# Kernel tuning notes

Hardware: AMD Instinct MI355X
Metric: run time of the kernel (lower is better)

Reference implementation:

```python
import jax, jax.numpy as jnp
from jax import lax
import numpy as np

NDIM = 256
BATCH = 65536
NROT = NDIM * (NDIM - 1) // 2  # comb(ndim, 2) = 32640


def _givens_mat(rots, ii, jj, ndim):
    """Product G_last @ ... @ G_1 of Givens rotations in combinations order.

    Left-multiplying by G(i, j, theta) only modifies rows i and j, so we apply
    each rotation as a rank-2 row update instead of a full matmul (same math
    as the original `plane_rot_mat @ mat` loop).
    """
    def step(mat, carry):
        i, j, th = carry
        c = jnp.cos(th)
        s = jnp.sin(th)
        ri = mat[i]
        rj = mat[j]
        mat = mat.at[i].set(c * ri - s * rj)
        mat = mat.at[j].set(s * ri + c * rj)
        return mat, None

    mat0 = jnp.eye(ndim, dtype=jnp.complex64)
    mat, _ = lax.scan(step, mat0, (ii, jj, rots))
    return mat


def setup_inputs() -> dict:
    key = jax.random.key(0)
    k1, k2, k3, k4 = jax.random.split(key, 4)
    x = jax.random.normal(k1, (BATCH, NDIM), dtype=jnp.float32)
    rots1 = 0.1 * jax.random.normal(k2, (NROT,), dtype=jnp.float32)
    phases = 0.1 * jax.random.normal(k3, (NDIM,), dtype=jnp.float32)
    rots2 = 0.1 * jax.random.normal(k4, (NROT,), dtype=jnp.float32)
    return {"x": x, "rots1": rots1, "phases": phases, "rots2": rots2}


def reference(x, rots1, phases, rots2):
    ndim = x.shape[1]
    # np.triu_indices(ndim, 1) enumerates (i, j) pairs in the same row-major
    # order as itertools.combinations(range(ndim), 2).
    ii_np, jj_np = np.triu_indices(ndim, k=1)
    ii = jnp.asarray(ii_np, dtype=jnp.int32)
    jj = jnp.asarray(jj_np, dtype=jnp.int32)

    # vector_norm: row-wise L2 normalization
    xn = x / jnp.linalg.norm(x, axis=1, keepdims=True)
    xc = xn.astype(jnp.complex64)

    # rot1: y = x @ M1.T with M1 = G_last @ ... @ G_1
    M1 = _givens_mat(rots1, ii, jj, ndim)
    y = xc @ M1.T

    # phase_transforms: x @ diag(exp(i*phases)) == elementwise phase multiply
    y = y * jnp.exp(1j * phases)

    # rot2
    M2 = _givens_mat(rots2, ii, jj, ndim)
    y = y @ M2.T

    # measure: |.|^2
    return jnp.abs(y) ** 2
```

## Files before the change

kernel.cpp:

```cpp
#include <hip/hip_runtime.h>
#include <stdint.h>
#include <math.h>

#define NDIM 256
#define BATCH 65536
#define NROT 32640

typedef float  f32x4 __attribute__((ext_vector_type(4)));
typedef short  s16x8 __attribute__((ext_vector_type(8)));
typedef unsigned int u32x4 __attribute__((ext_vector_type(4)));
typedef unsigned int u32x2 __attribute__((ext_vector_type(2)));

static __device__ __forceinline__ unsigned short f2bf(float f) {
    unsigned int u = __float_as_uint(f);
    u += 0x7fffu + ((u >> 16) & 1u);
    return (unsigned short)(u >> 16);
}
static __device__ __forceinline__ float bf2f(unsigned short h) {
    return __uint_as_float(((unsigned)h) << 16);
}

static __device__ __forceinline__ void split4(f32x4 v, u32x2* hi, u32x2* lo) {
    unsigned short h[4], l[4];
    #pragma unroll
    for (int i = 0; i < 4; i++) {
        h[i] = f2bf(v[i]);
        l[i] = f2bf(v[i] - bf2f(h[i]));
    }
    *hi = (u32x2){ (unsigned)h[0] | ((unsigned)h[1] << 16),
                   (unsigned)h[2] | ((unsigned)h[3] << 16) };
    *lo = (u32x2){ (unsigned)l[0] | ((unsigned)l[1] << 16),
                   (unsigned)l[2] | ((unsigned)l[3] << 16) };
}
static __device__ __forceinline__ void split8(const float* v, u32x4* hi, u32x4* lo) {
    unsigned short h[8], l[8];
    #pragma unroll
    for (int i = 0; i < 8; i++) {
        h[i] = f2bf(v[i]);
        l[i] = f2bf(v[i] - bf2f(h[i]));
    }
    *hi = (u32x4){ (unsigned)h[0] | ((unsigned)h[1] << 16),
                   (unsigned)h[2] | ((unsigned)h[3] << 16),
                   (unsigned)h[4] | ((unsigned)h[5] << 16),
                   (unsigned)h[6] | ((unsigned)h[7] << 16) };
    *lo = (u32x4){ (unsigned)l[0] | ((unsigned)l[1] << 16),
                   (unsigned)l[2] | ((unsigned)l[3] << 16),
                   (unsigned)l[4] | ((unsigned)l[5] << 16),
                   (unsigned)l[6] | ((unsigned)l[7] << 16) };
}

static __device__ __forceinline__ int sweep_bound(int k, int pblk) {
    int target = k * (NROT / pblk);
    int best = 0, bd = 0x7fffffff;
    for (int i = 0; i <= 256; i += 4) {
        int pre = i * 255 - (i * (i - 1)) / 2;
        int d = pre - target; d = (d < 0) ? -d : d;
        if (d < bd) { bd = d; best = i; }
    }
    return best;
}

__global__ __launch_bounds__(256) void k_cs(const float* __restrict__ r1,
                                            const float* __restrict__ r2,
                                            float2* __restrict__ cs) {
    int i = blockIdx.x * 256 + threadIdx.x;
    float th = (i < NROT) ? r1[i] : r2[i - NROT];
    float sv, cv; sincosf(th, &sv, &cv);
    cs[i] = make_float2(cv, sv);
}

__global__ __launch_bounds__(64) void k_blocks(const float2* __restrict__ cs,
                                               float* __restrict__ bmats, int pblk) {
    __shared__ float colb[264 * 64];
    __shared__ float2 csb[256 * 4];
    __shared__ float2 tri[24 * 6];

    const int t = threadIdx.x;
    const int bid = blockIdx.x;
    const int chunk = bid & 3;
    const int b = (bid >> 2) % pblk;
    const int set = (bid >> 2) / pblk;
    const int col0 = chunk * 64;
    const float2* cst = cs + (size_t)set * NROT;

    const int s0 = sweep_bound(b, pblk);
    const int s1 = sweep_bound(b + 1, pblk);
    const int ngroups = (s1 - s0) >> 2;

    {
        const f32x4 z = {0.f, 0.f, 0.f, 0.f};
        #pragma unroll 11
        for (int q = 0; q < 66; q++)
            *(f32x4*)&colb[(q * 64 + t) * 4] = z;
        colb[(col0 + t) * 64 + t] = 1.0f;
    }

    for (int k = t; k < ngroups * 6; k += 64) {
        int g = k / 6, q = k - g * 6;
        int a  = (q < 3) ? 0 : ((q < 5) ? 1 : 2);
        int bb = (q < 3) ? (q + 1) : ((q < 5) ? (q - 1) : 3);
        int m0 = s0 + g * 4;
        int m = m0 + a;
        int base = m * 255 - (m * (m - 1)) / 2;
        tri[k] = cst[base - m - 1 + m0 + bb];
    }

    for (int g = 0; g < ngroups; g++) {
        const int m0 = s0 + g * 4;
        int off[4];
        #pragma unroll
        for (int a = 0; a < 4; a++) {
            int m = m0 + a;
            int base = m * 255 - (m * (m - 1)) / 2;
            off[a] = base - m - 1;
        }
        const int n_j = 252 - m0;
        const int n_p = (n_j > 0) ? ((n_j + 7) & ~7) : 0;

        {
            const int kmax = n_p * 4;
            #pragma unroll 4
            for (int it = 0; it < 16; it++) {
                int k = t + it * 64;
                if (k < kmax) {
                    int jj = k >> 2, a = k & 3;
                    int j = m0 + 4 + jj;
                    csb[k] = (j < 256) ? cst[off[a] + j] : make_float2(1.f, 0.f);
                }
            }
        }

        float u0 = colb[(m0 + 0) * 64 + t];
        float u1 = colb[(m0 + 1) * 64 + t];
        float u2 = colb[(m0 + 2) * 64 + t];
        float u3 = colb[(m0 + 3) * 64 + t];

        {
            float2 cv; float nr;
            cv = tri[g * 6 + 0]; nr = cv.y * u0 + cv.x * u1; u0 = cv.x * u0 - cv.y * u1; u1 = nr;
            cv = tri[g * 6 + 1]; nr = cv.y * u0 + cv.x * u2; u0 = cv.x * u0 - cv.y * u2; u2 = nr;
            cv = tri[g * 6 + 2]; nr = cv.y * u0 + cv.x * u3; u0 = cv.x * u0 - cv.y * u3; u3 = nr;
            cv = tri[g * 6 + 3]; nr = cv.y * u1 + cv.x * u2; u1 = cv.x * u1 - cv.y * u2; u2 = nr;
            cv = tri[g * 6 + 4]; nr = cv.y * u1 + cv.x * u3; u1 = cv.x * u1 - cv.y * u3; u3 = nr;
            cv = tri[g * 6 + 5]; nr = cv.y * u2 + cv.x * u3; u2 = cv.x * u2 - cv.y * u3; u3 = nr;
        }

        if (n_p > 0) {
            float rbuf[8];
            #pragma unroll
            for (int p = 0; p < 8; p++)
                rbuf[p] = colb[(m0 + 4 + p) * 64 + t];
            for (int c = 0; c < n_p; c += 8) {
                #pragma unroll
                for (int p = 0; p < 8; p++) {
                    const int j = m0 + 4 + c + p;
                    float r = rbuf[p];
                    int jn = j + 8; jn = (jn < 263) ? jn : 263;
                    rbuf[p] = colb[jn * 64 + t];
                    float2 a0 = csb[(c + p) * 4 + 0];
                    float2 a1 = csb[(c + p) * 4 + 1];
                    float2 a2 = csb[(c + p) * 4 + 2];
                    float2 a3 = csb[(c + p) * 4 + 3];
                    float nr;
                    nr = a0.y * u0 + a0.x * r; u0 = a0.x * u0 - a0.y * r; r = nr;
                    nr = a1.y * u1 + a1.x * r; u1 = a1.x * u1 - a1.y * r; r = nr;
                    nr = a2.y * u2 + a2.x * r; u2 = a2.x * u2 - a2.y * r; r = nr;
                    nr = a3.y * u3 + a3.x * r; u3 = a3.x * u3 - a3.y * r; r = nr;
                    colb[j * 64 + t] = r;
                }
            }
        }
        colb[(m0 + 0) * 64 + t] = u0;
        colb[(m0 + 1) * 64 + t] = u1;
        colb[(m0 + 2) * 64 + t] = u2;
        colb[(m0 + 3) * 64 + t] = u3;
    }

    float* outm = bmats + (size_t)(set * pblk + b) * 65536;
    for (int r = 0; r < 256; r++)
        outm[(size_t)r * 256 + col0 + t] = colb[r * 64 + t];
}

__global__ __launch_bounds__(256) void k_combine(const float* __restrict__ src,
                                                 float* __restrict__ dst,
                                                 int half, int pblk,
                                                 const float* __restrict__ xg,
                                                 unsigned short* __restrict__ xbf) {
    const int by = blockIdx.y;
    const int tid = threadIdx.x;

    if (by >= 2 * half) {
        const int id = (by - 2 * half) * 16 + blockIdx.x;
        const int w = tid >> 6, lane = tid & 63;
        const int r0 = id * 64;
        #pragma unroll 2
        for (int p = 0; p < 16; p++) {
            int row = r0 + p * 4 + w;
            f32x4 v = *(const f32x4*)&xg[(size_t)row * 256 + lane * 4];
            float s = v[0] * v[0] + v[1] * v[1] + v[2] * v[2] + v[3] * v[3];
            #pragma unroll
            for (int off = 32; off; off >>= 1) s += __shfl_xor(s, off, 64);
            float sc = 1.0f / sqrtf(s);
            unsigned short h0 = f2bf(v[0] * sc), h1 = f2bf(v[1] * sc);
            unsigned short h2 = f2bf(v[2] * sc), h3 = f2bf(v[3] * sc);
            u32x2 pk = { (unsigned)h0 | ((unsigned)h1 << 16),
                         (unsigned)h2 | ((unsigned)h3 << 16) };
            *(u32x2*)&xbf[(size_t)row * 256 + lane * 4] = pk;
        }
        return;
    }

    const int set = by / half, pidx = by % half;
    const int stride = pblk / (2 * half);
    const int s0A = sweep_bound((2 * pidx + 1) * stride, pblk);
    const float* Am = src + (size_t)(set * 2 * half + 2 * pidx + 1) * 65536;
    const float* Bm = src + (size_t)(set * 2 * half + 2 * pidx) * 65536;
    float* Dm = dst + (size_t)(set * half + pidx) * 65536;
    const int tr = blockIdx.x >> 2, tc = blockIdx.x & 3;

    if (tr * 64 + 64 <= s0A) {
        #pragma unroll
        for (int it = 0; it < 4; it++) {
            int flat = tid + it * 256;
            int r = flat >> 4, c4 = flat & 15;
            size_t idx = (size_t)(tr * 64 + r) * 256 + tc * 64 + c4 * 4;
            *(f32x4*)&Dm[idx] = *(const f32x4*)&Bm[idx];
        }
        return;
    }
    const int kb0 = (tr * 64 >= s0A) ? (s0A >> 5) : 0;

    __shared__ unsigned short Ahi[64 * 40], Alo[64 * 40];
    __shared__ unsigned short Bhi[64 * 40], Blo[64 * 40];

    const int lane = tid & 63, w = tid >> 6;
    const int mh = (w >> 1) * 32, nh = (w & 1) * 32;
    const int l15 = lane & 15, lq = lane >> 4;
    const int bn = tid & 63, bkq = tid >> 6;

    f32x4 acc[2][2];
    #pragma unroll
    for (int i = 0; i < 2; i++)
        #pragma unroll
        for (int j = 0; j < 2; j++) acc[i][j] = (f32x4){0.f, 0.f, 0.f, 0.f};

    for (int kb = kb0; kb < 8; kb++) {
        __syncthreads();
        #pragma unroll
        for (int it = 0; it < 2; it++) {
            int flat = tid + it * 256;
            int r = flat >> 3, c4 = flat & 7;
            f32x4 v = *(const f32x4*)&Am[(size_t)(tr * 64 + r) * 256 + kb * 32 + c4 * 4];
            u32x2 hi, lo; split4(v, &hi, &lo);
            *(u32x2*)&Ahi[r * 40 + c4 * 4] = hi;
            *(u32x2*)&Alo[r * 40 + c4 * 4] = lo;
        }
        {
            float bv[8];
            #pragma unroll
            for (int i = 0; i < 8; i++)
                bv[i] = Bm[(size_t)(kb * 32 + bkq * 8 + i) * 256 + tc * 64 + bn];
            u32x4 hi, lo; split8(bv, &hi, &lo);
            *(u32x4*)&Bhi[bn * 40 + bkq * 8] = hi;
            *(u32x4*)&Blo[bn * 40 + bkq * 8] = lo;
        }
        __syncthreads();
        s16x8 ah[2], al[2], bh[2], bl[2];
        #pragma unroll
        for (int tm = 0; tm < 2; tm++) {
            ah[tm] = *(const s16x8*)&Ahi[(mh + tm * 16 + l15) * 40 + lq * 8];
            al[tm] = *(const s16x8*)&Alo[(mh + tm * 16 + l15) * 40 + lq * 8];
        }
        #pragma unroll
        for (int tn = 0; tn < 2; tn++) {
            bh[tn] = *(const s16x8*)&Bhi[(nh + tn * 16 + l15) * 40 + lq * 8];
            bl[tn] = *(const s16x8*)&Blo[(nh + tn * 16 + l15) * 40 + lq * 8];
        }
        #pragma unroll
        for (int tm = 0; tm < 2; tm++)
            #pragma unroll
            for (int tn = 0; tn < 2; tn++) {
                acc[tm][tn] = __builtin_amdgcn_mfma_f32_16x16x32_bf16(ah[tm], bh[tn], acc[tm][tn], 0, 0, 0);
                acc[tm][tn] = __builtin_amdgcn_mfma_f32_16x16x32_bf16(ah[tm], bl[tn], acc[tm][tn], 0, 0, 0);
                acc[tm][tn] = __builtin_amdgcn_mfma_f32_16x16x32_bf16(al[tm], bh[tn], acc[tm][tn], 0, 0, 0);
            }
    }
    #pragma unroll
    for (int tm = 0; tm < 2; tm++)
        #pragma unroll
        for (int tn = 0; tn < 2; tn++)
            #pragma unroll
            for (int r = 0; r < 4; r++)
                Dm[(size_t)(tr * 64 + mh + tm * 16 + lq * 4 + r) * 256
                   + tc * 64 + nh + tn * 16 + l15] = acc[tm][tn][r];
}

__global__ __launch_bounds__(256) void k_abt(const float* __restrict__ mats,
                                             const float* __restrict__ phases,
                                             unsigned short* __restrict__ abt) {
    const float* Am = mats + 65536;
    const float* Bm = mats;
    const int v = blockIdx.y;
    const int tr = blockIdx.x >> 2, tc = blockIdx.x & 3;
    const int tid = threadIdx.x;

    __shared__ unsigned short Ahi[64 * 40], Alo[64 * 40];
    __shared__ unsigned short Bhi[64 * 40], Blo[64 * 40];

    const int lane = tid & 63, w = tid >> 6;
    const int mh = (w >> 1) * 32, nh = (w & 1) * 32;
    const int l15 = lane & 15, lq = lane >> 4;
    const int bn = tid & 63, bkq = tid >> 6;

    f32x4 acc[2][2];
    #pragma unroll
    for (int i = 0; i < 2; i++)
        #pragma unroll
        for (int j = 0; j < 2; j++) acc[i][j] = (f32x4){0.f, 0.f, 0.f, 0.f};

    for (int kb = 0; kb < 8; kb++) {
        __syncthreads();
        #pragma unroll
        for (int it = 0; it < 2; it++) {
            int flat = tid + it * 256;
            int r = flat >> 3, c4 = flat & 7;
            f32x4 vv = *(const f32x4*)&Am[(size_t)(tr * 64 + r) * 256 + kb * 32 + c4 * 4];
            u32x2 hi, lo; split4(vv, &hi, &lo);
            *(u32x2*)&Ahi[r * 40 + c4 * 4] = hi;
            *(u32x2*)&Alo[r * 40 + c4 * 4] = lo;
        }
        {
            float bv[8];
            #pragma unroll
            for (int i = 0; i < 8; i++) {
                int kg = kb * 32 + bkq * 8 + i;
                float ph = phases[kg];
                float sc = v ? sinf(ph) : cosf(ph);
                bv[i] = Bm[(size_t)kg * 256 + tc * 64 + bn] * sc;
            }
            u32x4 hi, lo; split8(bv, &hi, &lo);
            *(u32x4*)&Bhi[bn * 40 + bkq * 8] = hi;
            *(u32x4*)&Blo[bn * 40 + bkq * 8] = lo;
        }
        __syncthreads();
        s16x8 ah[2], al[2], bh[2], bl[2];
        #pragma unroll
        for (int tm = 0; tm < 2; tm++) {
            ah[tm] = *(const s16x8*)&Ahi[(mh + tm * 16 + l15) * 40 + lq * 8];
            al[tm] = *(const s16x8*)&Alo[(mh + tm * 16 + l15) * 40 + lq * 8];
        }
        #pragma unroll
        for (int tn = 0; tn < 2; tn++) {
            bh[tn] = *(const s16x8*)&Bhi[(nh + tn * 16 + l15) * 40 + lq * 8];
            bl[tn] = *(const s16x8*)&Blo[(nh + tn * 16 + l15) * 40 + lq * 8];
        }
        #pragma unroll
        for (int tm = 0; tm < 2; tm++)
            #pragma unroll
            for (int tn = 0; tn < 2; tn++) {
                acc[tm][tn] = __builtin_amdgcn_mfma_f32_16x16x32_bf16(ah[tm], bh[tn], acc[tm][tn], 0, 0, 0);
                acc[tm][tn] = __builtin_amdgcn_mfma_f32_16x16x32_bf16(ah[tm], bl[tn], acc[tm][tn], 0, 0, 0);
                acc[tm][tn] = __builtin_amdgcn_mfma_f32_16x16x32_bf16(al[tm], bh[tn], acc[tm][tn], 0, 0, 0);
            }
    }
    #pragma unroll
    for (int tm = 0; tm < 2; tm++)
        #pragma unroll
        for (int tn = 0; tn < 2; tn++)
            #pragma unroll
            for (int r = 0; r < 4; r++)
                abt[(size_t)(v * 256 + tr * 64 + mh + tm * 16 + lq * 4 + r) * 256
                    + tc * 64 + nh + tn * 16 + l15] = f2bf(acc[tm][tn][r]);
}

__global__ __launch_bounds__(256) void k_norm(const float* __restrict__ x,
                                              float* __restrict__ invn) {
    const int row = blockIdx.x * 4 + (threadIdx.x >> 6);
    const int lane = threadIdx.x & 63;
    f32x4 v = *(const f32x4*)&x[(size_t)row * 256 + lane * 4];
    float s = v[0] * v[0] + v[1] * v[1] + v[2] * v[2] + v[3] * v[3];
    for (int off = 32; off; off >>= 1) s += __shfl_xor(s, off, 64);
    if (lane == 0) invn[row] = 1.0f / sqrtf(s);
}

#define BKP 136
__global__ __launch_bounds__(256) void k_gemm_bf(const unsigned short* __restrict__ xbf,
                                                 const unsigned short* __restrict__ abt,
                                                 float* __restrict__ out) {
    __shared__ unsigned short As[128 * BKP];
    __shared__ unsigned short Bs[128 * BKP];
    const int tid = threadIdx.x;
    const int cb = blockIdx.x;
    const int rb = blockIdx.y;
    const int lane = tid & 63, w = tid >> 6;

    f32x4 acc[16];
    #pragma unroll
    for (int i = 0; i < 16; i++) acc[i] = (f32x4){0.f, 0.f, 0.f, 0.f};

    int rA[8], cA[8], grB[8];
    #pragma unroll
    for (int it = 0; it < 8; it++) {
        int flat = tid + it * 256;
        rA[it] = flat >> 4; cA[it] = flat & 15;
        int r = rA[it];
        grB[it] = (r < 64) ? (cb * 64 + r) : (256 + cb * 64 + (r - 64));
    }

    u32x4 pa[8], pb[8];
    #pragma unroll
    for (int it = 0; it < 8; it++) {
        pa[it] = *(const u32x4*)&xbf[(size_t)(rb * 128 + rA[it]) * 256 + cA[it] * 8];
        pb[it] = *(const u32x4*)&abt[(size_t)grB[it] * 256 + cA[it] * 8];
    }
    #pragma unroll
    for (int it = 0; it < 8; it++) {
        *(u32x4*)&As[rA[it] * BKP + cA[it] * 8] = pa[it];
        *(u32x4*)&Bs[rA[it] * BKP + cA[it] * 8] = pb[it];
    }
    __syncthreads();
    #pragma unroll
    for (int it = 0; it < 8; it++) {
        pa[it] = *(const u32x4*)&xbf[(size_t)(rb * 128 + rA[it]) * 256 + 128 + cA[it] * 8];
        pb[it] = *(const u32x4*)&abt[(size_t)grB[it] * 256 + 128 + cA[it] * 8];
    }

    auto compute = [&]() {
        #pragma unroll
        for (int ks = 0; ks < 4; ks++) {
            const int k0 = ks * 32 + (lane >> 4) * 8;
            s16x8 a[2], b[8];
            #pragma unroll
            for (int tm = 0; tm < 2; tm++)
                a[tm] = *(const s16x8*)&As[(w * 32 + tm * 16 + (lane & 15)) * BKP + k0];
            #pragma unroll
            for (int tn = 0; tn < 8; tn++)
                b[tn] = *(const s16x8*)&Bs[(tn * 16 + (lane & 15)) * BKP + k0];
            #pragma unroll
            for (int tm = 0; tm < 2; tm++)
                #pragma unroll
                for (int tn = 0; tn < 8; tn++)
                    acc[tm * 8 + tn] = __builtin_amdgcn_mfma_f32_16x16x32_bf16(
                        a[tm], b[tn], acc[tm * 8 + tn], 0, 0, 0);
        }
    };
    compute();
    __syncthreads();
    #pragma unroll
    for (int it = 0; it < 8; it++) {
        *(u32x4*)&As[rA[it] * BKP + cA[it] * 8] = pa[it];
        *(u32x4*)&Bs[rA[it] * BKP + cA[it] * 8] = pb[it];
    }
    __syncthreads();
    compute();

    const int qr = lane >> 4, c = lane & 15;
    #pragma unroll
    for (int tm = 0; tm < 2; tm++) {
        #pragma unroll
        for (int tn = 0; tn < 4; tn++) {
            f32x4 p = acc[tm * 8 + tn];
            f32x4 q = acc[tm * 8 + tn + 4];
            #pragma unroll
            for (int r = 0; r < 4; r++) {
                int m = w * 32 + tm * 16 + qr * 4 + r;
                out[(size_t)(rb * 128 + m) * 256 + cb * 64 + tn * 16 + c] =
                    p[r] * p[r] + q[r] * q[r];
            }
        }
    }
}

__global__ __launch_bounds__(256) void k_gemm_f32(const float* __restrict__ x,
                                                  const unsigned short* __restrict__ abt,
                                                  const float* __restrict__ invn,
                                                  float* __restrict__ out) {
    __shared__ unsigned short As[128 * BKP];
    __shared__ unsigned short Bs[128 * BKP];
    const int tid = threadIdx.x;
    const int cb = blockIdx.x;
    const int rb = blockIdx.y;
    const int lane = tid & 63, w = tid >> 6;

    f32x4 acc[16];
    #pragma unroll
    for (int i = 0; i < 16; i++) acc[i] = (f32x4){0.f, 0.f, 0.f, 0.f};

    for (int kb = 0; kb < 2; kb++) {
        __syncthreads();
        #pragma unroll
        for (int it = 0; it < 16; it++) {
            int flat = tid + it * 256;
            int r = flat >> 5, c4 = flat & 31;
            f32x4 v = *(const f32x4*)&x[(size_t)(rb * 128 + r) * 256 + kb * 128 + c4 * 4];
            float sc = invn[rb * 128 + r];
            v[0] *= sc; v[1] *= sc; v[2] *= sc; v[3] *= sc;
            unsigned short h0 = f2bf(v[0]), h1 = f2bf(v[1]);
            unsigned short h2 = f2bf(v[2]), h3 = f2bf(v[3]);
            u32x2 pk = { (unsigned)h0 | ((unsigned)h1 << 16),
                         (unsigned)h2 | ((unsigned)h3 << 16) };
            *(u32x2*)&As[r * BKP + c4 * 4] = pk;
        }
        #pragma unroll
        for (int it = 0; it < 8; it++) {
            int flat = tid + it * 256;
            int r = flat >> 4, c8 = flat & 15;
            int gr = (r < 64) ? (cb * 64 + r) : (256 + cb * 64 + (r - 64));
            u32x4 vv = *(const u32x4*)&abt[(size_t)gr * 256 + kb * 128 + c8 * 8];
            *(u32x4*)&Bs[r * BKP + c8 * 8] = vv;
        }
        __syncthreads();
        #pragma unroll
        for (int ks = 0; ks < 4; ks++) {
            const int k0 = ks * 32 + (lane >> 4) * 8;
            s16x8 a[2], b[8];
            #pragma unroll
            for (int tm = 0; tm < 2; tm++)
                a[tm] = *(const s16x8*)&As[(w * 32 + tm * 16 + (lane & 15)) * BKP + k0];
            #pragma unroll
            for (int tn = 0; tn < 8; tn++)
                b[tn] = *(const s16x8*)&Bs[(tn * 16 + (lane & 15)) * BKP + k0];
            #pragma unroll
            for (int tm = 0; tm < 2; tm++)
                #pragma unroll
                for (int tn = 0; tn < 8; tn++)
                    acc[tm * 8 + tn] = __builtin_amdgcn_mfma_f32_16x16x32_bf16(
                        a[tm], b[tn], acc[tm * 8 + tn], 0, 0, 0);
        }
    }

    const int qr = lane >> 4, c = lane & 15;
    #pragma unroll
    for (int tm = 0; tm < 2; tm++) {
        #pragma unroll
        for (int tn = 0; tn < 4; tn++) {
            f32x4 p = acc[tm * 8 + tn];
            f32x4 q = acc[tm * 8 + tn + 4];
            #pragma unroll
            for (int r = 0; r < 4; r++) {
                int m = w * 32 + tm * 16 + qr * 4 + r;
                out[(size_t)(rb * 128 + m) * 256 + cb * 64 + tn * 16 + c] =
                    p[r] * p[r] + q[r] * q[r];
            }
        }
    }
}

extern "C" void kernel_launch(void* const* d_in, const int* in_sizes, int n_in,
                              void* d_out, int out_size, void* d_ws, size_t ws_size,
                              hipStream_t stream) {
    (void)in_sizes; (void)n_in; (void)out_size;
    const float* x      = (const float*)d_in[0];
    const float* rots1  = (const float*)d_in[1];
    const float* phases = (const float*)d_in[2];
    const float* rots2  = (const float*)d_in[3];
    float* out = (float*)d_out;
    char* ws = (char*)d_ws;

    const size_t MAT = 262144;
    int pblk = 32;
    while (pblk > 16 &&
           (size_t)3 * pblk * MAT + 2 * MAT + (size_t)BATCH * 512 > ws_size)
        pblk >>= 1;
    const size_t offA   = 0;
    const size_t offB   = offA + (size_t)2 * pblk * MAT;
    const size_t offABT = offB + (size_t)pblk * MAT;
    const size_t offINV = offABT + MAT;
    const size_t offXBF = offINV + MAT;
    const bool use_xbf = (offXBF + (size_t)BATCH * 512) <= ws_size;

    float*          A    = (float*)(ws + offA);
    float*          B    = (float*)(ws + offB);
    unsigned short* abt  = (unsigned short*)(ws + offABT);
    float*          invn = (float*)(ws + offINV);
    unsigned short* xbf  = (unsigned short*)(ws + offXBF);
    float2*         cs   = (float2*)(ws + offB);

    k_cs<<<(2 * NROT) / 256, 256, 0, stream>>>(rots1, rots2, cs);
    k_blocks<<<8 * pblk, 64, 0, stream>>>(cs, A, pblk);

    float* srcp = A; float* dstp = B;
    bool first = true;
    for (int half = pblk / 2; half >= 1; half >>= 1) {
        const int xny = (first && use_xbf) ? 64 : 0;
        k_combine<<<dim3(16, 2 * half + xny), 256, 0, stream>>>(srcp, dstp, half, pblk,
                                                                x, xbf);
        float* tmp = srcp; srcp = dstp; dstp = tmp;
        first = false;
    }
    k_abt<<<dim3(16, 2), 256, 0, stream>>>(srcp, phases, abt);

    if (use_xbf) {
        k_gemm_bf<<<dim3(4, BATCH / 128), 256, 0, stream>>>(xbf, abt, out);
    } else {
        k_norm<<<BATCH / 4, 256, 0, stream>>>(x, invn);
        k_gemm_f32<<<dim3(4, BATCH / 128), 256, 0, stream>>>(x, abt, invn, out);
    }
}
```

Measured before the change: 274.2 us.

## Double-buffer Givens coefficient staging and remap GEMM blocks across XCDs

In the block-building kernel, the cos/sin coefficients for the next group of four rows are loaded into registers from global memory while the current group is processed, then written into the alternate LDS buffer. This hides global load latency behind the rotation sweep. The inner loop now reads coefficients as vectorized f32x4 LDS loads, register-prefetched one step ahead. Both GEMM kernels remap block IDs so that consecutive blocks on the same XCD cover contiguous row tiles, which is meant to improve L2 locality. The extra register arrays raise register pressure, and the remap assumes a fixed grid of 4 by 512.

```diff
diff --git a/kernel.cpp b/kernel.cpp
--- a/kernel.cpp
+++ b/kernel.cpp
@@ -72,7 +72,7 @@
 __global__ __launch_bounds__(64) void k_blocks(const float2* __restrict__ cs,
                                                float* __restrict__ bmats, int pblk) {
     __shared__ float colb[264 * 64];
-    __shared__ float2 csb[256 * 4];
+    __shared__ float2 csb[2][256 * 4];
     __shared__ float2 tri[24 * 6];
 
     const int t = threadIdx.x;
@@ -105,28 +105,49 @@
         tri[k] = cst[base - m - 1 + m0 + bb];
     }
 
+    float2 gv[16];
+    {
+        const int m0g = s0;
+        int offg[4];
+        #pragma unroll
+        for (int a = 0; a < 4; a++) {
+            int m = m0g + a;
+            offg[a] = m * 255 - (m * (m - 1)) / 2 - m - 1;
+        }
+        #pragma unroll
+        for (int it = 0; it < 16; it++) {
+            int k = t + it * 64;
+            int jj = k >> 2, a = k & 3;
+            int j = m0g + 4 + jj;
+            gv[it] = (j < 256) ? cst[offg[a] + j] : make_float2(1.f, 0.f);
+        }
+        #pragma unroll
+        for (int it = 0; it < 16; it++)
+            csb[0][t + it * 64] = gv[it];
+    }
+
     for (int g = 0; g < ngroups; g++) {
         const int m0 = s0 + g * 4;
-        int off[4];
-        #pragma unroll
-        for (int a = 0; a < 4; a++) {
-            int m = m0 + a;
-            int base = m * 255 - (m * (m - 1)) / 2;
-            off[a] = base - m - 1;
-        }
+        const int buf = g & 1;
         const int n_j = 252 - m0;
         const int n_p = (n_j > 0) ? ((n_j + 7) & ~7) : 0;
-
-        {
-            const int kmax = n_p * 4;
-            #pragma unroll 4
+        const float* csbuf = (const float*)&csb[buf][0];
+
+        const bool have_next = (g + 1 < ngroups);
+        if (have_next) {
+            const int m0g = m0 + 4;
+            int offg[4];
+            #pragma unroll
+            for (int a = 0; a < 4; a++) {
+                int m = m0g + a;
+                offg[a] = m * 255 - (m * (m - 1)) / 2 - m - 1;
+            }
+            #pragma unroll
             for (int it = 0; it < 16; it++) {
                 int k = t + it * 64;
-                if (k < kmax) {
-                    int jj = k >> 2, a = k & 3;
-                    int j = m0 + 4 + jj;
-                    csb[k] = (j < 256) ? cst[off[a] + j] : make_float2(1.f, 0.f);
-                }
+                int jj = k >> 2, a = k & 3;
+                int j = m0g + 4 + jj;
+                gv[it] = (j < 256) ? cst[offg[a] + j] : make_float2(1.f, 0.f);
             }
         }
 
@@ -147,25 +168,29 @@
 
         if (n_p > 0) {
             float rbuf[8];
-            #pragma unroll
-            for (int p = 0; p < 8; p++)
+            f32x4 abuf[8][2];
+            #pragma unroll
+            for (int p = 0; p < 8; p++) {
                 rbuf[p] = colb[(m0 + 4 + p) * 64 + t];
+                abuf[p][0] = *(const f32x4*)&csbuf[p * 8 + 0];
+                abuf[p][1] = *(const f32x4*)&csbuf[p * 8 + 4];
+            }
             for (int c = 0; c < n_p; c += 8) {
                 #pragma unroll
                 for (int p = 0; p < 8; p++) {
                     const int j = m0 + 4 + c + p;
                     float r = rbuf[p];
+                    f32x4 A01 = abuf[p][0], A23 = abuf[p][1];
                     int jn = j + 8; jn = (jn < 263) ? jn : 263;
+                    int cn = c + p + 8; cn = (cn < n_p) ? cn : (n_p - 1);
                     rbuf[p] = colb[jn * 64 + t];
-                    float2 a0 = csb[(c + p) * 4 + 0];
-                    float2 a1 = csb[(c + p) * 4 + 1];
-                    float2 a2 = csb[(c + p) * 4 + 2];
-                    float2 a3 = csb[(c + p) * 4 + 3];
+                    abuf[p][0] = *(const f32x4*)&csbuf[cn * 8 + 0];
+                    abuf[p][1] = *(const f32x4*)&csbuf[cn * 8 + 4];
                     float nr;
-                    nr = a0.y * u0 + a0.x * r; u0 = a0.x * u0 - a0.y * r; r = nr;
-                    nr = a1.y * u1 + a1.x * r; u1 = a1.x * u1 - a1.y * r; r = nr;
-                    nr = a2.y * u2 + a2.x * r; u2 = a2.x * u2 - a2.y * r; r = nr;
-                    nr = a3.y * u3 + a3.x * r; u3 = a3.x * u3 - a3.y * r; r = nr;
+                    nr = A01[1] * u0 + A01[0] * r; u0 = A01[0] * u0 - A01[1] * r; r = nr;
+                    nr = A01[3] * u1 + A01[2] * r; u1 = A01[2] * u1 - A01[3] * r; r = nr;
+                    nr = A23[1] * u2 + A23[0] * r; u2 = A23[0] * u2 - A23[1] * r; r = nr;
+                    nr = A23[3] * u3 + A23[2] * r; u3 = A23[2] * u3 - A23[3] * r; r = nr;
                     colb[j * 64 + t] = r;
                 }
             }
@@ -174,6 +199,12 @@
         colb[(m0 + 1) * 64 + t] = u1;
         colb[(m0 + 2) * 64 + t] = u2;
         colb[(m0 + 3) * 64 + t] = u3;
+
+        if (have_next) {
+            #pragma unroll
+            for (int it = 0; it < 16; it++)
+                csb[buf ^ 1][t + it * 64] = gv[it];
+        }
     }
 
     float* outm = bmats + (size_t)(set * pblk + b) * 65536;
@@ -390,8 +421,10 @@
     __shared__ unsigned short As[128 * BKP];
     __shared__ unsigned short Bs[128 * BKP];
     const int tid = threadIdx.x;
-    const int cb = blockIdx.x;
-    const int rb = blockIdx.y;
+    const int l  = blockIdx.y * 4 + blockIdx.x;
+    const int L  = (l & 7) * 256 + (l >> 3);
+    const int cb = L & 3;
+    const int rb = L >> 2;
     const int lane = tid & 63, w = tid >> 6;
 
     f32x4 acc[16];
@@ -478,8 +511,10 @@
     __shared__ unsigned short As[128 * BKP];
     __shared__ unsigned short Bs[128 * BKP];
     const int tid = threadIdx.x;
-    const int cb = blockIdx.x;
-    const int rb = blockIdx.y;
+    const int l  = blockIdx.y * 4 + blockIdx.x;
+    const int L  = (l & 7) * 256 + (l >> 3);
+    const int cb = L & 3;
+    const int rb = L >> 2;
     const int lane = tid & 63, w = tid >> 6;
 
     f32x4 acc[16];
```

New measurement: 263.4 us. -4.0%, faster.
